# Performance work log

Hardware: AMD Instinct MI355X
Metric: run time of the kernel (lower is better)

The kernel has to match this reference:

```python
import jax, jax.numpy as jnp
import numpy as np

N = 100000
IN_F = 128
OUT_F = 128
E = 6400000


def setup_inputs() -> dict:
    key = jax.random.key(0)
    k1, k2, k3, k4, k5, k6 = jax.random.split(key, 6)
    layer_input = jax.random.normal(k1, (N, IN_F), dtype=jnp.float32)
    adj_rows = jax.random.randint(k2, (E,), 0, N, dtype=jnp.int64)
    adj_cols = jax.random.randint(k3, (E,), 0, N, dtype=jnp.int64)
    adj_vals = jax.random.uniform(k4, (E,), dtype=jnp.float32)
    # Linear params (torch default init scale ~ 1/sqrt(in_features))
    bound = 1.0 / np.sqrt(IN_F)
    W = jax.random.uniform(k5, (OUT_F, IN_F), minval=-bound, maxval=bound, dtype=jnp.float32)
    b = jax.random.uniform(k6, (OUT_F,), minval=-bound, maxval=bound, dtype=jnp.float32)
    return {"layer_input": layer_input, "adj_rows": adj_rows, "adj_cols": adj_cols,
            "adj_vals": adj_vals, "W": W, "b": b}


def reference(layer_input, adj_rows, adj_cols, adj_vals, W, b):
    # x = Linear(layer_input): [N, OUT_F]
    x = jnp.einsum('ni,oi->no', layer_input, W) + b
    # out = adj @ x  (sparse COO SpMM): out[r] += vals[e] * x[cols[e]]
    msgs = adj_vals[:, None] * x[adj_cols]  # [E, OUT_F]
    out = jax.ops.segment_sum(msgs, adj_rows, num_segments=N)
    return out
```

## Files before the change

kernel.cpp:

```cpp
#include <hip/hip_runtime.h>
#include <hip/hip_bf16.h>


#define BROWS 64
#define BSHIFT 6
#define CAPB 4608
#define CSHIFT 11
#define CROWS 2048
#define CAPC 135168
#define BPB 32
#define RGRID 1792
#define RMAX 14
#define NPAIRS 7
#define QUADS 4

typedef short bf16x8 __attribute__((ext_vector_type(8)));
typedef float f32x4 __attribute__((ext_vector_type(4)));
typedef unsigned u32x2 __attribute__((ext_vector_type(2)));
typedef unsigned u32x4 __attribute__((ext_vector_type(4)));

__device__ __forceinline__ unsigned pack_rn(float a, float b) {
  unsigned ua = __float_as_uint(a), ub = __float_as_uint(b);
  return ((ua + 0x8000u) >> 16) | ((ub + 0x8000u) & 0xFFFF0000u);
}

__device__ __forceinline__ unsigned quad_of(unsigned col) {
  return (col * 5242u) >> 27;
}

__global__ __launch_bounds__(256, 2) void gemm_mfma_kernel(
    const float* __restrict__ in, const float* __restrict__ W,
    const float* __restrict__ bias, unsigned* __restrict__ xbp, int N) {
  const int lane = threadIdx.x & 63;
  const int wv = threadIdx.x >> 6;
  const int m = lane & 15;
  const int kq = lane >> 4;
  bf16x8 bfr[4][8];
#pragma unroll
  for (int kk = 0; kk < 4; ++kk) {
#pragma unroll
    for (int nt = 0; nt < 8; ++nt) {
      const float* wp = W + (size_t)(nt * 16 + m) * 128 + kk * 32 + kq * 8;
      float4 w0 = *reinterpret_cast<const float4*>(wp);
      float4 w1 = *reinterpret_cast<const float4*>(wp + 4);
      uint4 u;
      u.x = pack_rn(w0.x, w0.y);
      u.y = pack_rn(w0.z, w0.w);
      u.z = pack_rn(w1.x, w1.y);
      u.w = pack_rn(w1.z, w1.w);
      bfr[kk][nt] = __builtin_bit_cast(bf16x8, u);
    }
  }
  float bl[8];
#pragma unroll
  for (int nt = 0; nt < 8; ++nt) bl[nt] = bias[nt * 16 + m];
  const int T = N >> 4;
  for (int t = blockIdx.x * 4 + wv; t < T; t += gridDim.x * 4) {
    const float* ap = in + (size_t)(t * 16 + m) * 128 + kq * 8;
    float4 xv[8];
#pragma unroll
    for (int kk = 0; kk < 4; ++kk) {
      xv[2 * kk] = *reinterpret_cast<const float4*>(ap + kk * 32);
      xv[2 * kk + 1] = *reinterpret_cast<const float4*>(ap + kk * 32 + 4);
    }
    f32x4 acc[8] = {};
#pragma unroll
    for (int kk = 0; kk < 4; ++kk) {
      uint4 u;
      u.x = pack_rn(xv[2 * kk].x, xv[2 * kk].y);
      u.y = pack_rn(xv[2 * kk].z, xv[2 * kk].w);
      u.z = pack_rn(xv[2 * kk + 1].x, xv[2 * kk + 1].y);
      u.w = pack_rn(xv[2 * kk + 1].z, xv[2 * kk + 1].w);
      bf16x8 af = __builtin_bit_cast(bf16x8, u);
#pragma unroll
      for (int nt = 0; nt < 8; ++nt)
        acc[nt] = __builtin_amdgcn_mfma_f32_16x16x32_bf16(af, bfr[kk][nt], acc[nt], 0, 0, 0);
    }
    unsigned* op = xbp + (size_t)(t * 16 + kq * 4) * 64 + m;
#pragma unroll
    for (int nt = 0; nt < 4; ++nt) {
#pragma unroll
      for (int j = 0; j < 4; ++j) {
        op[(size_t)j * 64 + nt * 16] =
            pack_rn(acc[nt][j] + bl[nt], acc[nt + 4][j] + bl[nt + 4]);
      }
    }
  }
}

__global__ void initcur_kernel(int* __restrict__ ccur, int nc,
                               int* __restrict__ fcur, int nfb) {
  int i = blockIdx.x * blockDim.x + threadIdx.x;
  if (i < nc) ccur[i] = i * CAPC;
  if (i < nfb) fcur[i] = i * CAPB;
}

__global__ __launch_bounds__(256) void scatterA_kernel(
    const int* __restrict__ rows, const int* __restrict__ cols,
    const float* __restrict__ vals, int* __restrict__ ccur,
    uint2* __restrict__ epackA, int E) {
  __shared__ int lhist[64];
  __shared__ int lbase[64];
  const int tid = threadIdx.x;
  const int E4 = E >> 2;
  const int per = (E4 + gridDim.x - 1) / gridDim.x;
  const int c0 = blockIdx.x * per;
  const int c1 = min(E4, c0 + per);
  const int4* rows4 = reinterpret_cast<const int4*>(rows);
  const int4* cols4 = reinterpret_cast<const int4*>(cols);
  const float4* vals4 = reinterpret_cast<const float4*>(vals);
  if (tid < 64) lhist[tid] = 0;
  __syncthreads();
  for (int i = c0 + tid; i < c1; i += 256) {
    int4 r4 = rows4[i];
    atomicAdd(&lhist[r4.x >> CSHIFT], 1);
    atomicAdd(&lhist[r4.y >> CSHIFT], 1);
    atomicAdd(&lhist[r4.z >> CSHIFT], 1);
    atomicAdd(&lhist[r4.w >> CSHIFT], 1);
  }
  __syncthreads();
  if (tid < 64) {
    int c = lhist[tid];
    lbase[tid] = c ? atomicAdd(&ccur[tid], c) : 0;
  }
  __syncthreads();
  for (int i = c0 + tid; i < c1; i += 256) {
    int4 r4 = rows4[i];
    int4 q4 = cols4[i];
    float4 v4 = vals4[i];
#define SCAT1(rr, cc, vv)                                                     \
    {                                                                         \
      int cb = (rr) >> CSHIFT;                                                \
      int p = atomicAdd(&lbase[cb], 1);                                       \
      if (p < (cb + 1) * CAPC)                                                \
        epackA[p] = make_uint2(                                               \
            ((unsigned)((rr) & (CROWS - 1)) << 17) | (unsigned)(cc),          \
            __float_as_uint(vv));                                             \
    }
    SCAT1(r4.x, q4.x, v4.x)
    SCAT1(r4.y, q4.y, v4.y)
    SCAT1(r4.z, q4.z, v4.z)
    SCAT1(r4.w, q4.w, v4.w)
#undef SCAT1
  }
}

__global__ __launch_bounds__(256) void scatterB_kernel(
    const int* __restrict__ ccur, const uint2* __restrict__ epackA,
    int* __restrict__ fcur, unsigned* __restrict__ epackB) {
  __shared__ int lhist[32];
  __shared__ int lbase[32];
  const int c = blockIdx.x / BPB;
  const int sub = blockIdx.x % BPB;
  const int tid = threadIdx.x;
  const int base = c * CAPC;
  int cnt = ccur[c] - base;
  if (cnt > CAPC) cnt = CAPC;
  const int s0 = base + (int)((long long)cnt * sub / BPB);
  const int s1 = base + (int)((long long)cnt * (sub + 1) / BPB);
  if (tid < 32) lhist[tid] = 0;
  __syncthreads();
  for (int i = s0 + tid; i < s1; i += 256)
    atomicAdd(&lhist[epackA[i].x >> 23], 1);
  __syncthreads();
  if (tid < 32) {
    int n = lhist[tid];
    lbase[tid] = n ? atomicAdd(&fcur[(c << 5) + tid], n) : 0;
  }
  __syncthreads();
  for (int i = s0 + tid; i < s1; i += 256) {
    uint2 e = epackA[i];
    int fb = e.x >> 23;
    int gfb = (c << 5) + fb;
    int p = atomicAdd(&lbase[fb], 1);
    unsigned q = (unsigned)__builtin_rintf(__uint_as_float(e.y) * 511.0f);
    if (p < (gfb + 1) * CAPB)
      epackB[p] = (q << 23) | (e.x & 0x7FFFFFu);
  }
}

__global__ __launch_bounds__(256) void rowsort6_kernel(
    const int* __restrict__ fcur, const unsigned* __restrict__ epackB,
    unsigned* __restrict__ ered, unsigned* __restrict__ scT, int N) {
  __shared__ unsigned ebuf[CAPB];
  __shared__ int cnt256[QUADS * 64];
  __shared__ int cbase256[QUADS * 64];
  __shared__ int qtot[QUADS], qbase[QUADS];
  const int b = blockIdx.x;
  const int base = b * CAPB;
  int m = fcur[b] - base;
  if (m > CAPB) m = CAPB;
  const int tid = threadIdx.x;
  if (tid < QUADS * 64) cnt256[tid] = 0;
  __syncthreads();
  const u32x4* ep4 = reinterpret_cast<const u32x4*>(epackB + base);
  const int mp = m >> 2;
  for (int i4 = tid; i4 < mp; i4 += 256) {
    u32x4 four = ep4[i4];
    ebuf[4 * i4] = four.x;
    ebuf[4 * i4 + 1] = four.y;
    ebuf[4 * i4 + 2] = four.z;
    ebuf[4 * i4 + 3] = four.w;
    atomicAdd(&cnt256[(quad_of(four.x & 0x1FFFFu) << 6) | ((four.x >> 17) & 63u)], 1);
    atomicAdd(&cnt256[(quad_of(four.y & 0x1FFFFu) << 6) | ((four.y >> 17) & 63u)], 1);
    atomicAdd(&cnt256[(quad_of(four.z & 0x1FFFFu) << 6) | ((four.z >> 17) & 63u)], 1);
    atomicAdd(&cnt256[(quad_of(four.w & 0x1FFFFu) << 6) | ((four.w >> 17) & 63u)], 1);
  }
  if (tid == 0) {
    for (int i = m & ~3; i < m; ++i) {
      unsigned e = epackB[base + i];
      ebuf[i] = e;
      atomicAdd(&cnt256[(quad_of(e & 0x1FFFFu) << 6) | ((e >> 17) & 63u)], 1);
    }
  }
  __syncthreads();
  if (tid < QUADS) {
    int s = 0;
    for (int r = 0; r < 64; ++r) {
      cbase256[(tid << 6) | r] = s;
      s += cnt256[(tid << 6) | r];
    }
    qtot[tid] = s;
  }
  __syncthreads();
  if (tid == 0) {
    int run = 0;
    for (int o = 0; o < QUADS; ++o) { qbase[o] = run; run += qtot[o]; }
  }
  __syncthreads();
  if (tid < QUADS) {
    int ob = qbase[tid];
    for (int r = 0; r < 64; ++r) cbase256[(tid << 6) | r] += ob;
  }
  __syncthreads();
  const int rbase = b << BSHIFT;
  if (tid < 64 && rbase + tid < N) {
    for (int o = 0; o < QUADS; ++o) {
      unsigned st = (unsigned)(base + cbase256[(o << 6) | tid]);
      unsigned ct = (unsigned)min(cnt256[(o << 6) | tid], 511);
      scT[(size_t)o * N + rbase + tid] = (st << 9) | ct;
    }
  }
  __syncthreads();
  for (int i = tid; i < m; i += 256) {
    unsigned e = ebuf[i];
    unsigned col = e & 0x1FFFFu;
    int p = atomicAdd(&cbase256[(quad_of(col) << 6) | ((e >> 17) & 63u)], 1);
    ered[base + p] = ((e >> 23) << 17) | col;
  }
}

__global__ __launch_bounds__(256, 7) void reduce9e_kernel(
    const unsigned* __restrict__ scT, const unsigned* __restrict__ ered,
    const unsigned* __restrict__ xbp, float* __restrict__ out, int N) {
  const int lane = threadIdx.x & 63;
  const int lp = lane & 31;
  const int half = lane >> 5;
  const int w = blockIdx.x * 4 + (threadIdx.x >> 6);
  const int nwaves = RGRID * 4;
  const int brows = N / nwaves;
  const int extra = N - brows * nwaves;
  const int rbase = w * brows + min(w, extra);
  const int nrows = brows + (w < extra ? 1 : 0);
  const float S = 1.0f / (511.0f * 131072.0f);
  const char* xb = (const char*)xbp;
  const unsigned laneb = (unsigned)(lp << 3);
  const int halfb4 = half << 7;
  float a0[NPAIRS], a1[NPAIRS], a2[NPAIRS], a3[NPAIRS];
#pragma unroll
  for (int p = 0; p < NPAIRS; ++p) { a0[p] = 0.f; a1[p] = 0.f; a2[p] = 0.f; a3[p] = 0.f; }

#define PAIR(jj)                                                              \
  {                                                                           \
    int idx4 = halfb4 + ((jj) << 2);                                          \
    int o_ = __builtin_amdgcn_ds_bpermute(idx4, (int)vo);                     \
    int vb_ = __builtin_amdgcn_ds_bpermute(idx4, __float_as_int(vv));         \
    u32x2 u_ = *(const u32x2*)(xb + (size_t)(unsigned)(o_ + (int)laneb));     \
    float v_ = __int_as_float(vb_);                                           \
    a0[p] += v_ * __uint_as_float(u_.x << 16);                                \
    a1[p] += v_ * __uint_as_float(u_.x & 0xFFFF0000u);                        \
    a2[p] += v_ * __uint_as_float(u_.y << 16);                                \
    a3[p] += v_ * __uint_as_float(u_.y & 0xFFFF0000u);                        \
  }

  for (int oct = 0; oct < QUADS; ++oct) {
    unsigned scv = 0;
    if (lane < nrows) scv = scT[(size_t)oct * N + rbase + lane];
#pragma unroll
    for (int p = 0; p < NPAIRS; ++p) {
      const unsigned scvA = (unsigned)__builtin_amdgcn_readlane((int)scv, 2 * p);
      const unsigned scvB = (unsigned)__builtin_amdgcn_readlane((int)scv, 2 * p + 1);
      const int sA = (int)(scvA >> 9), nA = (int)(scvA & 511u);
      const int sB = (int)(scvB >> 9), nB = (int)(scvB & 511u);
      const int s_my = half ? sB : sA;
      const int n_my = half ? nB : nA;
      const int nmax = max(nA, nB);
      for (int off = 0; off < nmax; off += 32) {
        const int rel = off + lp;
        unsigned ew = 0;
        if (rel < n_my) ew = ered[s_my + rel];
        float vv = (float)ew;
        unsigned vo = (ew & 0x1FFFFu) << 8;
        int m2 = nmax - off;
        if (m2 > 32) m2 = 32;
        int j = 0;
        for (; j + 4 <= m2; j += 4) {
          PAIR(j) PAIR(j + 1) PAIR(j + 2) PAIR(j + 3)
        }
        for (; j < m2; ++j) PAIR(j)
      }
    }
  }
#undef PAIR
#pragma unroll
  for (int p = 0; p < NPAIRS; ++p) {
    if (2 * p + half < nrows) {
      const int r = rbase + 2 * p + half;
      float* op = out + (size_t)r * 128 + 2 * lp;
      float2 lo2 = make_float2(a0[p] * S, a2[p] * S);
      float2 hi2 = make_float2(a1[p] * S, a3[p] * S);
      *reinterpret_cast<float2*>(op) = lo2;
      *reinterpret_cast<float2*>(op + 64) = hi2;
    }
  }
}

extern "C" void kernel_launch(void* const* d_in, const int* in_sizes, int n_in,
                              void* d_out, int out_size, void* d_ws, size_t ws_size,
                              hipStream_t stream) {
  const float* layer_input = (const float*)d_in[0];
  const int* adj_rows = (const int*)d_in[1];
  const int* adj_cols = (const int*)d_in[2];
  const float* adj_vals = (const float*)d_in[3];
  const float* W = (const float*)d_in[4];
  const float* bias = (const float*)d_in[5];
  float* out = (float*)d_out;
  const int N = in_sizes[0] / 128;
  const int E = in_sizes[1];
  const int nc = (N + CROWS - 1) >> CSHIFT;
  const int nfb = nc << 5;
  const int nb = (N + BROWS - 1) >> BSHIFT;

  char* ws = (char*)d_ws;
  size_t off = 0;
  unsigned* xbp = (unsigned*)(ws + off);       off += (size_t)N * 64 * 4;
  int* ccur = (int*)(ws + off);                off += ((size_t)nc * 4 + 255) & ~255ull;
  int* fcur = (int*)(ws + off);                off += ((size_t)nfb * 4 + 255) & ~255ull;
  unsigned* scT = (unsigned*)(ws + off);       off += ((size_t)8 * N * 4 + 255) & ~255ull;
  unsigned* epackB = (unsigned*)(ws + off);    off += (size_t)nfb * CAPB * 4;
  uint2* epackA = (uint2*)(ws + off);
  unsigned* ered = (unsigned*)epackA;
  off += (size_t)nc * CAPC * 8;

  initcur_kernel<<<(nfb + 255) / 256, 256, 0, stream>>>(ccur, nc, fcur, nfb);
  gemm_mfma_kernel<<<512, 256, 0, stream>>>(layer_input, W, bias, xbp, N);
  scatterA_kernel<<<1024, 256, 0, stream>>>(adj_rows, adj_cols, adj_vals, ccur, epackA, E);
  scatterB_kernel<<<nc * BPB, 256, 0, stream>>>(ccur, epackA, fcur, epackB);
  rowsort6_kernel<<<nb, 256, 0, stream>>>(fcur, epackB, ered, scT, N);
  reduce9e_kernel<<<RGRID, 256, 0, stream>>>(scT, ered, xbp, out, N);
}
```

Baseline: 302.7 us.

## Process four rows per wave with 16-byte gathers in reduce kernel

The reduction kernel now splits each wave into four 16-lane quarters, each handling one row, instead of two 32-lane halves. Each lane gathers 16 bytes (8 bf16 features) per edge rather than 8 bytes, so each row's 256-byte feature vector is read by 16 lanes. The aim is fewer gather instructions and fewer iterations per edge batch, plus more rows in flight per wave. In exchange it takes more accumulator registers per group, and load imbalance across four rows in the max-count loop can waste lanes. With 16 rows per wave as NG=4, the RMAX coverage of 14 rows is still met.

```diff
diff --git a/kernel.cpp b/kernel.cpp
--- a/kernel.cpp
+++ b/kernel.cpp
@@ -11,7 +11,7 @@
 #define BPB 32
 #define RGRID 1792
 #define RMAX 14
-#define NPAIRS 7
+#define NG 4
 #define QUADS 4
 
 typedef short bf16x8 __attribute__((ext_vector_type(8)));
@@ -250,12 +250,14 @@
   }
 }
 
-__global__ __launch_bounds__(256, 7) void reduce9e_kernel(
+__global__ __launch_bounds__(256, 7) void reduce11_kernel(
     const unsigned* __restrict__ scT, const unsigned* __restrict__ ered,
     const unsigned* __restrict__ xbp, float* __restrict__ out, int N) {
   const int lane = threadIdx.x & 63;
-  const int lp = lane & 31;
-  const int half = lane >> 5;
+  const int lp16 = lane & 15;
+  const int q = lane >> 4;
+  const int qb4 = (lane & 48) << 2;
+  const int qsel = (lane & 48) >> 2;
   const int w = blockIdx.x * 4 + (threadIdx.x >> 6);
   const int nwaves = RGRID * 4;
   const int brows = N / nwaves;
@@ -264,63 +266,70 @@
   const int nrows = brows + (w < extra ? 1 : 0);
   const float S = 1.0f / (511.0f * 131072.0f);
   const char* xb = (const char*)xbp;
-  const unsigned laneb = (unsigned)(lp << 3);
-  const int halfb4 = half << 7;
-  float a0[NPAIRS], a1[NPAIRS], a2[NPAIRS], a3[NPAIRS];
-#pragma unroll
-  for (int p = 0; p < NPAIRS; ++p) { a0[p] = 0.f; a1[p] = 0.f; a2[p] = 0.f; a3[p] = 0.f; }
-
-#define PAIR(jj)                                                              \
+  const unsigned laneb = (unsigned)(lp16 << 4);
+  float aL0[NG], aL1[NG], aL2[NG], aL3[NG];
+  float aH0[NG], aH1[NG], aH2[NG], aH3[NG];
+#pragma unroll
+  for (int g = 0; g < NG; ++g) {
+    aL0[g] = 0.f; aL1[g] = 0.f; aL2[g] = 0.f; aL3[g] = 0.f;
+    aH0[g] = 0.f; aH1[g] = 0.f; aH2[g] = 0.f; aH3[g] = 0.f;
+  }
+
+#define EDGE4(jj)                                                             \
   {                                                                           \
-    int idx4 = halfb4 + ((jj) << 2);                                          \
+    int idx4 = qb4 | ((jj) << 2);                                             \
     int o_ = __builtin_amdgcn_ds_bpermute(idx4, (int)vo);                     \
-    int vb_ = __builtin_amdgcn_ds_bpermute(idx4, __float_as_int(vv));         \
-    u32x2 u_ = *(const u32x2*)(xb + (size_t)(unsigned)(o_ + (int)laneb));     \
-    float v_ = __int_as_float(vb_);                                           \
-    a0[p] += v_ * __uint_as_float(u_.x << 16);                                \
-    a1[p] += v_ * __uint_as_float(u_.x & 0xFFFF0000u);                        \
-    a2[p] += v_ * __uint_as_float(u_.y << 16);                                \
-    a3[p] += v_ * __uint_as_float(u_.y & 0xFFFF0000u);                        \
+    float v_ = __int_as_float(                                                \
+        __builtin_amdgcn_ds_bpermute(idx4, __float_as_int(vv)));              \
+    u32x4 u_ = *(const u32x4*)(xb + (size_t)(unsigned)(o_ + (int)laneb));     \
+    aL0[g] += v_ * __uint_as_float(u_.x << 16);                               \
+    aH0[g] += v_ * __uint_as_float(u_.x & 0xFFFF0000u);                       \
+    aL1[g] += v_ * __uint_as_float(u_.y << 16);                               \
+    aH1[g] += v_ * __uint_as_float(u_.y & 0xFFFF0000u);                       \
+    aL2[g] += v_ * __uint_as_float(u_.z << 16);                               \
+    aH2[g] += v_ * __uint_as_float(u_.z & 0xFFFF0000u);                       \
+    aL3[g] += v_ * __uint_as_float(u_.w << 16);                               \
+    aH3[g] += v_ * __uint_as_float(u_.w & 0xFFFF0000u);                       \
   }
 
   for (int oct = 0; oct < QUADS; ++oct) {
     unsigned scv = 0;
     if (lane < nrows) scv = scT[(size_t)oct * N + rbase + lane];
 #pragma unroll
-    for (int p = 0; p < NPAIRS; ++p) {
-      const unsigned scvA = (unsigned)__builtin_amdgcn_readlane((int)scv, 2 * p);
-      const unsigned scvB = (unsigned)__builtin_amdgcn_readlane((int)scv, 2 * p + 1);
-      const int sA = (int)(scvA >> 9), nA = (int)(scvA & 511u);
-      const int sB = (int)(scvB >> 9), nB = (int)(scvB & 511u);
-      const int s_my = half ? sB : sA;
-      const int n_my = half ? nB : nA;
-      const int nmax = max(nA, nB);
-      for (int off = 0; off < nmax; off += 32) {
-        const int rel = off + lp;
+    for (int g = 0; g < NG; ++g) {
+      unsigned scq = (unsigned)__builtin_amdgcn_ds_bpermute(
+          (g << 4) | qsel, (int)scv);
+      const int s_my = (int)(scq >> 9);
+      const int n_my = (int)(scq & 511u);
+      int nm = n_my;
+      nm = max(nm, __shfl_xor(nm, 16));
+      nm = max(nm, __shfl_xor(nm, 32));
+      for (int off = 0; off < nm; off += 16) {
+        const int rel = off + lp16;
         unsigned ew = 0;
         if (rel < n_my) ew = ered[s_my + rel];
         float vv = (float)ew;
         unsigned vo = (ew & 0x1FFFFu) << 8;
-        int m2 = nmax - off;
-        if (m2 > 32) m2 = 32;
+        int m2 = nm - off;
+        if (m2 > 16) m2 = 16;
         int j = 0;
         for (; j + 4 <= m2; j += 4) {
-          PAIR(j) PAIR(j + 1) PAIR(j + 2) PAIR(j + 3)
+          EDGE4(j) EDGE4(j + 1) EDGE4(j + 2) EDGE4(j + 3)
         }
-        for (; j < m2; ++j) PAIR(j)
+        for (; j < m2; ++j) EDGE4(j)
       }
     }
   }
-#undef PAIR
-#pragma unroll
-  for (int p = 0; p < NPAIRS; ++p) {
-    if (2 * p + half < nrows) {
-      const int r = rbase + 2 * p + half;
-      float* op = out + (size_t)r * 128 + 2 * lp;
-      float2 lo2 = make_float2(a0[p] * S, a2[p] * S);
-      float2 hi2 = make_float2(a1[p] * S, a3[p] * S);
-      *reinterpret_cast<float2*>(op) = lo2;
-      *reinterpret_cast<float2*>(op + 64) = hi2;
+#undef EDGE4
+#pragma unroll
+  for (int g = 0; g < NG; ++g) {
+    if (4 * g + q < nrows) {
+      const int r = rbase + 4 * g + q;
+      float* op = out + (size_t)r * 128 + 4 * lp16;
+      f32x4 lo = {aL0[g] * S, aL1[g] * S, aL2[g] * S, aL3[g] * S};
+      f32x4 hi = {aH0[g] * S, aH1[g] * S, aH2[g] * S, aH3[g] * S};
+      *reinterpret_cast<f32x4*>(op) = lo;
+      *reinterpret_cast<f32x4*>(op + 64) = hi;
     }
   }
 }
@@ -357,5 +366,5 @@
   scatterA_kernel<<<1024, 256, 0, stream>>>(adj_rows, adj_cols, adj_vals, ccur, epackA, E);
   scatterB_kernel<<<nc * BPB, 256, 0, stream>>>(ccur, epackA, fcur, epackB);
   rowsort6_kernel<<<nb, 256, 0, stream>>>(fcur, epackB, ered, scT, N);
-  reduce9e_kernel<<<RGRID, 256, 0, stream>>>(scT, ered, xbp, out, N);
-}
+  reduce11_kernel<<<RGRID, 256, 0, stream>>>(scT, ered, xbp, out, N);
+}
```

New measurement: 324.4 us. +7.1%, slower.
